# Optimization experiments

Hardware: AMD Instinct MI355X
Metric: run time of the kernel (lower is better)

## Reference

```python
import jax, jax.numpy as jnp
import numpy as np

B, T, D, E = 4, 2048, 1024, 4096


def setup_inputs() -> dict:
    key = jax.random.key(0)
    ks = jax.random.split(key, 6)
    s = 0.02
    return {
        "x": jax.random.normal(ks[0], (B, T, D), jnp.float32),
        "W1": jax.random.normal(ks[1], (E, D), jnp.float32) * s,
        "b1": jnp.zeros((E,), jnp.float32),
        "W2": jax.random.normal(ks[2], (E, D), jnp.float32) * s,
        "b2": jnp.zeros((E,), jnp.float32),
        "Wg": jax.random.normal(ks[3], (2 * E, E), jnp.float32) * s,
        "bg": jnp.zeros((2 * E,), jnp.float32),
        "Wo": jax.random.normal(ks[4], (D, E), jnp.float32) * s,
        "bo": jnp.zeros((D,), jnp.float32),
    }


def _log_g(x):
    # log of g(x) where g(x) = x+0.5 for x>=0 else sigmoid(x)
    return jnp.where(x >= 0, jnp.log(jax.nn.relu(x) + 0.5), -jax.nn.softplus(-x))


def _min_gru(x_in, Wg, bg):
    # x_in: [B,T,E]; single linear -> (gate, candidate), log-space parallel scan, h0 = 0
    gh = jnp.einsum('bte,fe->btf', x_in, Wg) + bg
    gate, hidden = jnp.split(gh, 2, axis=-1)
    log_coeffs = -jax.nn.softplus(gate)          # log(1 - z)
    log_z = -jax.nn.softplus(-gate)              # log z
    log_values = log_z + _log_g(hidden)          # log(z * g(h_tilde))
    a_star = jnp.cumsum(log_coeffs, axis=1)      # Heinsen associative scan
    log_h = a_star + jax.lax.cumlogsumexp(log_values - a_star, axis=1)
    return jnp.exp(log_h)


def reference(x, W1, b1, W2, b2, Wg, bg, Wo, bo):
    x_in = jax.nn.silu(jnp.einsum('btd,ed->bte', x, W1) + b1)
    x_skip = jax.nn.silu(jnp.einsum('btd,ed->bte', x, W2) + b2)
    h = _min_gru(x_in, Wg, bg)
    return jnp.einsum('bte,de->btd', x_skip + h, Wo) + bo
```

## Files before the change

kernel.cpp:

```cpp
#include <hip/hip_runtime.h>
#include <cstdint>
#include <cstddef>

constexpr int CB  = 4;
constexpr int CT  = 2048;
constexpr int CD  = 1024;
constexpr int CE  = 4096;
constexpr int CM  = CB * CT;
constexpr int CN2E = 2 * CE;
constexpr int NCHUNK = 32;
constexpr int CLEN = CT / NCHUNK;

typedef float  f32x4   __attribute__((ext_vector_type(4)));
typedef __bf16 bf16x8  __attribute__((ext_vector_type(8)));

__device__ __forceinline__ unsigned short f2bf(float f) {
  unsigned int u = __float_as_uint(f);
  unsigned int r = u + 0x7FFFu + ((u >> 16) & 1u);
  return (unsigned short)(r >> 16);
}
__device__ __forceinline__ float bf2f(unsigned short h) {
  return __uint_as_float(((unsigned int)h) << 16);
}

__global__ __launch_bounds__(256) void k_f2bf4(const float* __restrict__ in,
                                               unsigned short* __restrict__ out, int n4) {
  int i = blockIdx.x * 256 + threadIdx.x;
  if (i >= n4) return;
  float4 v = ((const float4*)in)[i];
  ushort4 o;
  o.x = f2bf(v.x); o.y = f2bf(v.y); o.z = f2bf(v.z); o.w = f2bf(v.w);
  ((ushort4*)out)[i] = o;
}

__device__ __forceinline__ void gll16(const unsigned short* g, void* l) {
  __builtin_amdgcn_global_load_lds(
      (const __attribute__((address_space(1))) void*)g,
      (__attribute__((address_space(3))) void*)l, 16, 0, 0);
}

template <int EPI, int K>
__global__ __launch_bounds__(512, 2) void gemm256(
    const unsigned short* __restrict__ A,
    const unsigned short* __restrict__ Bw,
    const float* __restrict__ bias0,
    const float* __restrict__ bias1,
    void* __restrict__ out0,
    void* __restrict__ out1,
    int M, int N, int lda, int ld0, int esplit) {
  extern __shared__ char lds[];

  const int nbn = N >> 8;
  const int nbm = M >> 8;
  const int nwg = nbm * nbn;
  int bid = blockIdx.x;
  int tau = (bid & 7) * (nwg >> 3) + (bid >> 3);
  const int gsz = nbm * 4;
  int gg  = tau / gsz;
  int rem = tau - gg * gsz;
  const int bm = rem >> 2;
  const int bn = gg * 4 + (rem & 3);

  const int tid  = threadIdx.x;
  const int lane = tid & 63;
  const int wv   = tid >> 6;
  const int wr   = wv >> 2;
  const int wc   = wv & 3;

  const int sr2 = tid >> 2;
  const int scA = (((tid & 3) ^ ((sr2 >> 1) & 3)) * 8);

  const unsigned short* Abase = A  + (size_t)bm * 256 * lda;
  const unsigned short* Bbase = Bw + (size_t)bn * 256 * (size_t)K;
  constexpr int NT = K >> 6;
  const int ldsw = wv * 1024;

  auto stage = [&](const unsigned short* Xb, int ldx, int xoff, int t, int ks) {
    char* base = lds + (t & 1) * 65536 + xoff + ks * 16384 + ldsw;
    const unsigned short* g = Xb + (size_t)t * 64 + ks * 32 + scA;
    gll16(g + (size_t)sr2 * ldx, base);
    gll16(g + (size_t)(sr2 + 128) * ldx, base + 8192);
  };

  const int lr = lane & 15, lk = lane >> 4;
  const int rch = (lk ^ ((lr >> 1) & 3)) * 16;
  const int aB = (wr * 128 + lr) * 64 + rch;
  const int bB = 32768 + (wc * 64 + lr) * 64 + rch;

  f32x4 acc[8][4];
#pragma unroll
  for (int m = 0; m < 8; m++)
#pragma unroll
    for (int n = 0; n < 4; n++) acc[m][n] = (f32x4){0.f, 0.f, 0.f, 0.f};

  stage(Abase, lda, 0, 0, 0); stage(Bbase, K, 32768, 0, 0);
  stage(Abase, lda, 0, 0, 1); stage(Bbase, K, 32768, 0, 1);
  asm volatile("s_waitcnt vmcnt(4)" ::: "memory");
  __builtin_amdgcn_sched_barrier(0);
  __builtin_amdgcn_s_barrier();

#pragma unroll 2
  for (int t = 0; t < NT; t++) {
    const char* bp = lds + (t & 1) * 65536;
    bf16x8 bfr[4], aq[4];
#pragma unroll
    for (int ph = 0; ph < 4; ph++) {
      const int ks = ph >> 1, mh = ph & 1;
      const int ksb = ks * 16384;
#pragma unroll
      for (int i = 0; i < 4; i++)
        aq[i] = *(const bf16x8*)(bp + ksb + aB + (mh * 4 + i) * 1024);
      if (mh == 0) {
#pragma unroll
        for (int nf = 0; nf < 4; nf++)
          bfr[nf] = *(const bf16x8*)(bp + ksb + bB + nf * 1024);
      }
      if (t + 1 < NT) {
        if      (ph == 0) stage(Abase, lda, 0,     t + 1, 0);
        else if (ph == 1) stage(Bbase, K,   32768, t + 1, 0);
        else if (ph == 2) stage(Abase, lda, 0,     t + 1, 1);
        else              stage(Bbase, K,   32768, t + 1, 1);
      }
      __builtin_amdgcn_s_barrier();
      asm volatile("s_waitcnt lgkmcnt(0)" ::: "memory");
      __builtin_amdgcn_sched_barrier(0);
      __builtin_amdgcn_s_setprio(1);
#pragma unroll
      for (int i = 0; i < 4; i++)
#pragma unroll
        for (int nf = 0; nf < 4; nf++)
          acc[mh * 4 + i][nf] = __builtin_amdgcn_mfma_f32_16x16x32_bf16(
              aq[i], bfr[nf], acc[mh * 4 + i][nf], 0, 0, 0);
      __builtin_amdgcn_s_setprio(0);
      if (mh == 1) {
        if (t + 1 < NT) asm volatile("s_waitcnt vmcnt(4)" ::: "memory");
        else if (ks == 0) asm volatile("s_waitcnt vmcnt(0)" ::: "memory");
        __builtin_amdgcn_sched_barrier(0);
      }
      __builtin_amdgcn_s_barrier();
    }
  }

  const int rb = bm * 256 + wr * 128 + (lane >> 4) * 4;
  const int cb = bn * 256 + wc * 64 + (lane & 15);
#pragma unroll
  for (int nf = 0; nf < 4; nf++) {
    const int col = cb + nf * 16;
    float bi;
    if (EPI == 0) bi = (col < esplit) ? bias0[col] : bias1[col - esplit];
    else          bi = bias0[col];
#pragma unroll
    for (int mf = 0; mf < 8; mf++) {
#pragma unroll
      for (int r = 0; r < 4; r++) {
        const int row = rb + mf * 16 + r;
        float v = acc[mf][nf][r] + bi;
        if (EPI == 0) {
          float sg = 1.f / (1.f + __expf(-v));
          unsigned short o = f2bf(v * sg);
          if (col < esplit) ((unsigned short*)out0)[(size_t)row * ld0 + col] = o;
          else              ((unsigned short*)out1)[(size_t)row * ld0 + (col - esplit)] = o;
        } else if (EPI == 1) {
          ((float*)out0)[(size_t)row * ld0 + col] = v;
        } else {
          unsigned short o;
          if (col < esplit) {
            float e = __expf(-fabsf(v));
            float inv = 1.f / (1.f + e);
            o = f2bf((v >= 0.f) ? e * inv : inv);
          } else {
            float gf;
            if (v >= 0.f) gf = v + 0.5f;
            else { float eh = __expf(v); gf = eh / (1.f + eh); }
            o = f2bf(gf);
          }
          ((unsigned short*)out0)[(size_t)row * ld0 + col] = o;
        }
      }
    }
  }
}

__global__ __launch_bounds__(256) void k_scan1(const unsigned short* __restrict__ ghc,
                                               float* __restrict__ Ac,
                                               float* __restrict__ Bc) {
  int tid = threadIdx.x;
  int lane = tid & 63, cw = tid >> 6;
  int bid = blockIdx.x;
  int eg = bid & 63;
  int cq = bid >> 6;
  int chunk = cq * 4 + cw;
  int e = eg * 64 + lane;
  const unsigned short* cp = ghc + (size_t)(chunk * CLEN) * CN2E + e;
  float h = 0.f, A = 1.f;
#pragma unroll 8
  for (int t = 0; t < CLEN; t++) {
    float c  = bf2f(cp[(size_t)t * CN2E]);
    float gf = bf2f(cp[(size_t)t * CN2E + CE]);
    float v  = (1.f - c) * gf;
    h = __builtin_fmaf(c, h, v);
    A *= c;
  }
  Ac[(size_t)chunk * CE + e] = A;
  Bc[(size_t)chunk * CE + e] = h;
}

__global__ __launch_bounds__(256) void k_scan2(const float* __restrict__ Ac,
                                               const float* __restrict__ Bc,
                                               float* __restrict__ Hs) {
  int e = blockIdx.x * 256 + threadIdx.x;
  float h = 0.f;
#pragma unroll
  for (int ch = 0; ch < NCHUNK; ch++) {
    Hs[(size_t)ch * CE + e] = h;
    h = __builtin_fmaf(Ac[(size_t)ch * CE + e], h, Bc[(size_t)ch * CE + e]);
  }
}

__global__ __launch_bounds__(256) void k_scan3(const unsigned short* __restrict__ ghc,
                                               const float* __restrict__ Hs,
                                               const unsigned short* __restrict__ xs,
                                               unsigned short* __restrict__ sp) {
  int tid = threadIdx.x;
  int lane = tid & 63, cw = tid >> 6;
  int bid = blockIdx.x;
  int eg = bid & 63;
  int cq = bid >> 6;
  int chunk = cq * 4 + cw;
  int e = eg * 64 + lane;
  float h = Hs[(size_t)chunk * CE + e];
  const unsigned short* cp  = ghc + (size_t)(chunk * CLEN) * CN2E + e;
  const unsigned short* xsp = xs  + (size_t)(chunk * CLEN) * CE + e;
  unsigned short*       spp = sp  + (size_t)(chunk * CLEN) * CE + e;
#pragma unroll 4
  for (int t = 0; t < CLEN; t++) {
    float c  = bf2f(cp[(size_t)t * CN2E]);
    float gf = bf2f(cp[(size_t)t * CN2E + CE]);
    float v  = (1.f - c) * gf;
    h = __builtin_fmaf(c, h, v);
    float s = h + bf2f(xsp[(size_t)t * CE]);
    spp[(size_t)t * CE] = f2bf(s);
  }
}

extern "C" void kernel_launch(void* const* d_in, const int* in_sizes, int n_in,
                              void* d_out, int out_size, void* d_ws, size_t ws_size,
                              hipStream_t stream) {
  const float* x  = (const float*)d_in[0];
  const float* W1 = (const float*)d_in[1];
  const float* b1 = (const float*)d_in[2];
  const float* W2 = (const float*)d_in[3];
  const float* b2 = (const float*)d_in[4];
  const float* Wg = (const float*)d_in[5];
  const float* bg = (const float*)d_in[6];
  const float* Wo = (const float*)d_in[7];
  const float* bo = (const float*)d_in[8];
  float* out = (float*)d_out;

  const size_t MB = 1024 * 1024;
  if (ws_size < 234 * MB) return;
  char* ws = (char*)d_ws;
  unsigned short* wgb   = (unsigned short*)(ws);
  unsigned short* wob   = (unsigned short*)(ws + 64 * MB);
  unsigned short* wcat  = (unsigned short*)(ws + 72 * MB);
  unsigned short* xb    = (unsigned short*)(ws + 88 * MB);
  unsigned short* ghc   = (unsigned short*)(ws + 72 * MB);
  unsigned short* xin   = (unsigned short*)(ws + 104 * MB);
  unsigned short* xskip = (unsigned short*)(ws + 168 * MB);
  float* Ac = (float*)(ws + 232 * MB);
  float* Bc = (float*)(ws + 232 * MB + 512 * 1024);
  float* Hs = (float*)(ws + 233 * MB);

  hipFuncSetAttribute(reinterpret_cast<const void*>(&gemm256<0, CD>),
                      hipFuncAttributeMaxDynamicSharedMemorySize, 131072);
  hipFuncSetAttribute(reinterpret_cast<const void*>(&gemm256<1, CE>),
                      hipFuncAttributeMaxDynamicSharedMemorySize, 131072);
  hipFuncSetAttribute(reinterpret_cast<const void*>(&gemm256<2, CE>),
                      hipFuncAttributeMaxDynamicSharedMemorySize, 131072);

  {
    int n4;
    n4 = CM * CD / 4;   k_f2bf4<<<n4 / 256, 256, 0, stream>>>(x,  xb,   n4);
    n4 = CE * CD / 4;   k_f2bf4<<<n4 / 256, 256, 0, stream>>>(W1, wcat, n4);
    n4 = CE * CD / 4;   k_f2bf4<<<n4 / 256, 256, 0, stream>>>(W2, wcat + (size_t)CE * CD, n4);
    n4 = CN2E * CE / 4; k_f2bf4<<<n4 / 256, 256, 0, stream>>>(Wg, wgb,  n4);
    n4 = CD * CE / 4;   k_f2bf4<<<n4 / 256, 256, 0, stream>>>(Wo, wob,  n4);
  }

  gemm256<0, CD><<<(CM / 256) * (CN2E / 256), 512, 131072, stream>>>(
      xb, wcat, b1, b2, xin, xskip, CM, CN2E, CD, CE, CE);

  for (int b = 0; b < CB; b++) {
    const unsigned short* xin_b = xin + (size_t)b * CT * CE;
    gemm256<2, CE><<<(CT / 256) * (CN2E / 256), 512, 131072, stream>>>(
        xin_b, wgb, bg, nullptr, ghc, nullptr, CT, CN2E, CE, CN2E, CE);
    k_scan1<<<512, 256, 0, stream>>>(ghc, Ac, Bc);
    k_scan2<<<CE / 256, 256, 0, stream>>>(Ac, Bc, Hs);
    k_scan3<<<512, 256, 0, stream>>>(ghc, Hs, xskip + (size_t)b * CT * CE,
                                     xin + (size_t)b * CT * CE);
  }

  gemm256<1, CE><<<(CM / 256) * (CD / 256), 512, 131072, stream>>>(
      xin, wob, bo, nullptr, out, nullptr, CM, CD, CE, CD, 0);
}
```

Before: 959.8 us.

## Issue all next-tile loads early and merge per-batch gate GEMMs when workspace allows

```diff
diff --git a/kernel.cpp b/kernel.cpp
--- a/kernel.cpp
+++ b/kernel.cpp
@@ -116,10 +116,8 @@
           bfr[nf] = *(const bf16x8*)(bp + ksb + bB + nf * 1024);
       }
       if (t + 1 < NT) {
-        if      (ph == 0) stage(Abase, lda, 0,     t + 1, 0);
-        else if (ph == 1) stage(Bbase, K,   32768, t + 1, 0);
-        else if (ph == 2) stage(Abase, lda, 0,     t + 1, 1);
-        else              stage(Bbase, K,   32768, t + 1, 1);
+        if (ph == 0) { stage(Abase, lda, 0, t + 1, 0); stage(Bbase, K, 32768, t + 1, 0); }
+        if (ph == 1) { stage(Abase, lda, 0, t + 1, 1); stage(Bbase, K, 32768, t + 1, 1); }
       }
       __builtin_amdgcn_s_barrier();
       asm volatile("s_waitcnt lgkmcnt(0)" ::: "memory");
@@ -132,9 +130,13 @@
           acc[mh * 4 + i][nf] = __builtin_amdgcn_mfma_f32_16x16x32_bf16(
               aq[i], bfr[nf], acc[mh * 4 + i][nf], 0, 0, 0);
       __builtin_amdgcn_s_setprio(0);
-      if (mh == 1) {
-        if (t + 1 < NT) asm volatile("s_waitcnt vmcnt(4)" ::: "memory");
-        else if (ks == 0) asm volatile("s_waitcnt vmcnt(0)" ::: "memory");
+      if (ph == 1) {
+        if (t + 1 < NT) asm volatile("s_waitcnt vmcnt(8)" ::: "memory");
+        else            asm volatile("s_waitcnt vmcnt(0)" ::: "memory");
+        __builtin_amdgcn_sched_barrier(0);
+      }
+      if (ph == 3 && t + 1 < NT) {
+        asm volatile("s_waitcnt vmcnt(4)" ::: "memory");
         __builtin_amdgcn_sched_barrier(0);
       }
       __builtin_amdgcn_s_barrier();
@@ -260,16 +262,33 @@
   const size_t MB = 1024 * 1024;
   if (ws_size < 234 * MB) return;
   char* ws = (char*)d_ws;
-  unsigned short* wgb   = (unsigned short*)(ws);
-  unsigned short* wob   = (unsigned short*)(ws + 64 * MB);
-  unsigned short* wcat  = (unsigned short*)(ws + 72 * MB);
-  unsigned short* xb    = (unsigned short*)(ws + 88 * MB);
-  unsigned short* ghc   = (unsigned short*)(ws + 72 * MB);
-  unsigned short* xin   = (unsigned short*)(ws + 104 * MB);
-  unsigned short* xskip = (unsigned short*)(ws + 168 * MB);
-  float* Ac = (float*)(ws + 232 * MB);
-  float* Bc = (float*)(ws + 232 * MB + 512 * 1024);
-  float* Hs = (float*)(ws + 233 * MB);
+
+  const bool merged = (ws_size >= 332 * MB);
+  unsigned short *wgb, *wob, *wcat, *xb, *ghc, *xin, *xskip;
+  float *Ac, *Bc, *Hs;
+  if (merged) {
+    wgb   = (unsigned short*)(ws);
+    wob   = (unsigned short*)(ws + 64 * MB);
+    xin   = (unsigned short*)(ws + 72 * MB);
+    xskip = (unsigned short*)(ws + 136 * MB);
+    ghc   = (unsigned short*)(ws + 200 * MB);
+    wcat  = (unsigned short*)(ws + 200 * MB);
+    xb    = (unsigned short*)(ws + 216 * MB);
+    Ac = (float*)(ws + 328 * MB);
+    Bc = (float*)(ws + 328 * MB + 512 * 1024);
+    Hs = (float*)(ws + 329 * MB);
+  } else {
+    wgb   = (unsigned short*)(ws);
+    wob   = (unsigned short*)(ws + 64 * MB);
+    wcat  = (unsigned short*)(ws + 72 * MB);
+    xb    = (unsigned short*)(ws + 88 * MB);
+    ghc   = (unsigned short*)(ws + 72 * MB);
+    xin   = (unsigned short*)(ws + 104 * MB);
+    xskip = (unsigned short*)(ws + 168 * MB);
+    Ac = (float*)(ws + 232 * MB);
+    Bc = (float*)(ws + 232 * MB + 512 * 1024);
+    Hs = (float*)(ws + 233 * MB);
+  }
 
   hipFuncSetAttribute(reinterpret_cast<const void*>(&gemm256<0, CD>),
                       hipFuncAttributeMaxDynamicSharedMemorySize, 131072);
@@ -290,14 +309,26 @@
   gemm256<0, CD><<<(CM / 256) * (CN2E / 256), 512, 131072, stream>>>(
       xb, wcat, b1, b2, xin, xskip, CM, CN2E, CD, CE, CE);
 
-  for (int b = 0; b < CB; b++) {
-    const unsigned short* xin_b = xin + (size_t)b * CT * CE;
-    gemm256<2, CE><<<(CT / 256) * (CN2E / 256), 512, 131072, stream>>>(
-        xin_b, wgb, bg, nullptr, ghc, nullptr, CT, CN2E, CE, CN2E, CE);
-    k_scan1<<<512, 256, 0, stream>>>(ghc, Ac, Bc);
-    k_scan2<<<CE / 256, 256, 0, stream>>>(Ac, Bc, Hs);
-    k_scan3<<<512, 256, 0, stream>>>(ghc, Hs, xskip + (size_t)b * CT * CE,
-                                     xin + (size_t)b * CT * CE);
+  if (merged) {
+    gemm256<2, CE><<<(CM / 256) * (CN2E / 256), 512, 131072, stream>>>(
+        xin, wgb, bg, nullptr, ghc, nullptr, CM, CN2E, CE, CN2E, CE);
+    for (int b = 0; b < CB; b++) {
+      const unsigned short* ghc_b = ghc + (size_t)b * CT * CN2E;
+      k_scan1<<<512, 256, 0, stream>>>(ghc_b, Ac, Bc);
+      k_scan2<<<CE / 256, 256, 0, stream>>>(Ac, Bc, Hs);
+      k_scan3<<<512, 256, 0, stream>>>(ghc_b, Hs, xskip + (size_t)b * CT * CE,
+                                       xin + (size_t)b * CT * CE);
+    }
+  } else {
+    for (int b = 0; b < CB; b++) {
+      const unsigned short* xin_b = xin + (size_t)b * CT * CE;
+      gemm256<2, CE><<<(CT / 256) * (CN2E / 256), 512, 131072, stream>>>(
+          xin_b, wgb, bg, nullptr, ghc, nullptr, CT, CN2E, CE, CN2E, CE);
+      k_scan1<<<512, 256, 0, stream>>>(ghc, Ac, Bc);
+      k_scan2<<<CE / 256, 256, 0, stream>>>(Ac, Bc, Hs);
+      k_scan3<<<512, 256, 0, stream>>>(ghc, Hs, xskip + (size_t)b * CT * CE,
+                                       xin + (size_t)b * CT * CE);
+    }
   }
 
   gemm256<1, CE><<<(CM / 256) * (CD / 256), 512, 131072, stream>>>(
```

Measured after the change: 1.081 ms. 1.13x slower.
